# Optimization experiments

Hardware: AMD Instinct MI355X
Metric: run time of the kernel (lower is better)

## Reference

```python
import jax, jax.numpy as jnp
import numpy as np

REG = 0.1  # config['reg']


def _poly_filter(s, gammas):
    # Horner evaluation of sum_k gammas[k] * s**k (monomial basis, depth K=len-1).
    out = jnp.full_like(s, gammas[-1])
    for k in range(gammas.shape[0] - 2, -1, -1):
        out = out * s + gammas[k]
    return out


def setup_inputs() -> dict:
    key = jax.random.key(0)
    k1, k2, k3, k4, k5 = jax.random.split(key, 5)
    B, H, N, R = 4, 8, 4096, 64
    U = jax.random.normal(k1, (B, H, N, R), dtype=jnp.float32)
    Sigma = jax.random.normal(k2, (B, H, 1, R), dtype=jnp.float32)
    svd_V = jax.random.normal(k3, (B, H, N, R), dtype=jnp.float32)
    V = jax.random.normal(k4, (B, H, N, R), dtype=jnp.float32)
    mask = jnp.ones((B, N), dtype=jnp.float32)
    # learnable polynomial coefficients; gamma_0 fixed to 1 (fixI=True)
    gammas = jnp.concatenate([jnp.ones((1,), jnp.float32),
                              0.1 * jax.random.normal(k5, (4,), dtype=jnp.float32)])
    return {"U": U, "Sigma": Sigma, "svd_V": svd_V, "V": V, "mask": mask, "gammas": gammas}


def reference(U, Sigma, svd_V, V, mask, gammas):
    # Q: softmax over rank dim r
    Q = jax.nn.softmax(U, axis=-1)                                      # [B,H,N,r]
    # K: masked softmax over sequence dim N
    Kmat = jax.nn.softmax(svd_V - 1e9 * (1.0 - mask[:, None, :, None]), axis=-2)
    S = jax.nn.sigmoid(Sigma)                                           # [B,H,1,r]
    graph_filter = _poly_filter(S, gammas)                              # [B,H,1,r]
    # linear-attention ordering: (Q*filt) @ (K^T @ V), never forms NxN
    KtV = jnp.einsum('bhnr,bhnd->bhrd', Kmat, V)                        # [B,H,r,d]
    X = jnp.einsum('bhnr,bhrd->bhnd', Q * graph_filter, KtV)            # [B,H,N,d]
    r = Q.shape[-1]
    eye = jnp.eye(r, dtype=Q.dtype)
    symQ = jnp.einsum('bhnr,bhns->bhrs', Q, Q) - eye
    ortho_loss = REG * jnp.mean(jnp.abs(symQ), axis=(1, 2, 3))
    symK = jnp.einsum('bhnr,bhns->bhrs', Kmat, Kmat) - eye
    ortho_loss = ortho_loss + REG * jnp.mean(jnp.abs(symK), axis=(1, 2, 3))
    return X, ortho_loss
```

## Files before the change

### kernel.cpp

```cpp
#include <hip/hip_runtime.h>
#include <math.h>

#define NB 4
#define NH 8
#define BHN 32
#define SN 4096
#define RR 64
#define REGC 0.1f

#define MCH 16
#define MROWS 256
#define XCH 32
#define XROWS 128

typedef short s16x8 __attribute__((ext_vector_type(8)));
typedef float f32x4 __attribute__((ext_vector_type(4)));

__device__ __forceinline__ float wave_sum(float v) {
    #pragma unroll
    for (int off = 32; off; off >>= 1) v += __shfl_xor(v, off, 64);
    return v;
}
__device__ __forceinline__ unsigned short f2bf(float x) {
    unsigned int u = __float_as_uint(x);
    u += 0x7FFFu + ((u >> 16) & 1u);
    return (unsigned short)(u >> 16);
}
__device__ __forceinline__ float bf2f(unsigned short h) {
    return __uint_as_float(((unsigned int)h) << 16);
}
__device__ __forceinline__ unsigned int packbf(float a, float b) {
    return (unsigned int)f2bf(a) | ((unsigned int)f2bf(b) << 16);
}
__device__ __forceinline__ s16x8 ldfrag(const unsigned int* p) {
    uint4 r = *(const uint4*)p;
    return __builtin_bit_cast(s16x8, r);
}
__device__ __forceinline__ int swz(int row, int blk) {
    return (row << 5) + (((blk ^ (row & 7))) << 2);
}
__device__ __forceinline__ void split8(const float* x, uint4& hi, uint4& lo) {
    unsigned short h[8];
    #pragma unroll
    for (int i = 0; i < 8; i++) h[i] = f2bf(x[i]);
    hi = make_uint4((unsigned)h[0] | ((unsigned)h[1] << 16),
                    (unsigned)h[2] | ((unsigned)h[3] << 16),
                    (unsigned)h[4] | ((unsigned)h[5] << 16),
                    (unsigned)h[6] | ((unsigned)h[7] << 16));
    lo = make_uint4(packbf(x[0] - bf2f(h[0]), x[1] - bf2f(h[1])),
                    packbf(x[2] - bf2f(h[2]), x[3] - bf2f(h[3])),
                    packbf(x[4] - bf2f(h[4]), x[5] - bf2f(h[5])),
                    packbf(x[6] - bf2f(h[6]), x[7] - bf2f(h[7])));
}

__global__ void k_zero_loss(float* loss) {
    if (threadIdx.x < NB) loss[threadIdx.x] = 0.0f;
}

#define PH 0
#define VH 2048
#define VL 4096
#define QH 6144
__launch_bounds__(512, 4)
__global__ void k_main(const float* __restrict__ U, const float* __restrict__ sv,
                       const float* __restrict__ V, const float* __restrict__ mask,
                       float* __restrict__ ktv_part, float* __restrict__ symk_part,
                       float* __restrict__ symq_part, float* __restrict__ colsum_part) {
    __shared__ __align__(16) unsigned int sm[16384];
    const int chunk = blockIdx.x, bh = blockIdx.y, b = bh >> 3;
    const int t = threadIdx.x, l = t & 63, w = t >> 6;
    const int r15 = l & 15, quad = l >> 4;
    const int ni = w & 3, mi0 = (w >> 2) << 1;
    const size_t rowbase = (size_t)bh * SN * RR;
    const int row0 = chunk * MROWS;

    float csum = 0.0f;
    f32x4 aKV[2], aSK[2], aSQ[2];
    #pragma unroll
    for (int j = 0; j < 2; j++) {
        aKV[j] = (f32x4){0.f, 0.f, 0.f, 0.f};
        aSK[j] = (f32x4){0.f, 0.f, 0.f, 0.f};
        aSQ[j] = (f32x4){0.f, 0.f, 0.f, 0.f};
    }

    float bu[2][8], bx[2][8], bv[2][8];
    #pragma unroll
    for (int i = 0; i < 8; i++) {
        const size_t off = rowbase + (size_t)(row0 + 8 * w + i) * RR + l;
        bu[0][i] = U[off]; bx[0][i] = sv[off]; bv[0][i] = V[off];
    }

    #pragma unroll
    for (int s = 0; s < 4; s++) {
        const int cur = s & 1, nxt = cur ^ 1;
        const int nb = row0 + s * 64;
        const int bufb = (s & 1) * 8192;
        float bm[8];
        #pragma unroll
        for (int i = 0; i < 8; i++) bm[i] = mask[b * SN + nb + 8 * w + i];
        float q[8], p[8], vv[8];
        #pragma unroll
        for (int i = 0; i < 8; i++) {
            const float eu = __expf(bu[cur][i]);
            q[i] = eu * (1.0f / wave_sum(eu));
        }
        #pragma unroll
        for (int i = 0; i < 8; i++) {
            p[i] = __expf(bx[cur][i] - 1e9f * (1.0f - bm[i]));
            csum += p[i];
            vv[i] = bv[cur][i];
        }
        if (s < 3) {
            #pragma unroll
            for (int i = 0; i < 8; i++) {
                const size_t off = rowbase + (size_t)(nb + 64 + 8 * w + i) * RR + l;
                bu[nxt][i] = U[off]; bx[nxt][i] = sv[off]; bv[nxt][i] = V[off];
            }
        }
        uint4 vh, vl;
        split8(vv, vh, vl);
        const uint4 ph = make_uint4(packbf(p[0], p[1]), packbf(p[2], p[3]),
                                    packbf(p[4], p[5]), packbf(p[6], p[7]));
        const uint4 qh = make_uint4(packbf(q[0], q[1]), packbf(q[2], q[3]),
                                    packbf(q[4], q[5]), packbf(q[6], q[7]));
        const int wbase = bufb + (l << 5) + ((w ^ (l & 7)) << 2);
        *(uint4*)(sm + PH + wbase) = ph;
        *(uint4*)(sm + VH + wbase) = vh;
        *(uint4*)(sm + VL + wbase) = vl;
        *(uint4*)(sm + QH + wbase) = qh;
        __syncthreads();
        #pragma unroll
        for (int ks = 0; ks < 2; ks++) {
            const int ub = ks * 4 + quad;
            s16x8 Ah[2], AQ[2];
            #pragma unroll
            for (int j = 0; j < 2; j++) {
                const int oa = bufb + swz((mi0 + j) * 16 + r15, ub);
                Ah[j] = ldfrag(sm + PH + oa);
                AQ[j] = ldfrag(sm + QH + oa);
            }
            const int ob = bufb + swz(ni * 16 + r15, ub);
            const s16x8 Bvh = ldfrag(sm + VH + ob);
            const s16x8 Bvl = ldfrag(sm + VL + ob);
            const s16x8 Bph = ldfrag(sm + PH + ob);
            const s16x8 Bq  = ldfrag(sm + QH + ob);
            #pragma unroll
            for (int j = 0; j < 2; j++) {
                aKV[j] = __builtin_amdgcn_mfma_f32_16x16x32_bf16(Ah[j], Bvh, aKV[j], 0, 0, 0);
                aKV[j] = __builtin_amdgcn_mfma_f32_16x16x32_bf16(Ah[j], Bvl, aKV[j], 0, 0, 0);
                aSK[j] = __builtin_amdgcn_mfma_f32_16x16x32_bf16(Ah[j], Bph, aSK[j], 0, 0, 0);
                aSQ[j] = __builtin_amdgcn_mfma_f32_16x16x32_bf16(AQ[j], Bq,  aSQ[j], 0, 0, 0);
            }
        }
    }
    const size_t pb = ((size_t)bh * MCH + chunk) * 4096;
    #pragma unroll
    for (int j = 0; j < 2; j++)
        #pragma unroll
        for (int r = 0; r < 4; r++) {
            const int e = ((mi0 + j) * 16 + quad * 4 + r) * 64 + ni * 16 + r15;
            ktv_part[pb + e]  = aKV[j][r];
            symk_part[pb + e] = aSK[j][r];
            symq_part[pb + e] = aSQ[j][r];
        }
    __syncthreads();
    float* smf = (float*)sm;
    smf[w * 64 + l] = csum;
    __syncthreads();
    if (w == 0) {
        float scol = 0.f;
        #pragma unroll
        for (int j = 0; j < 8; j++) scol += smf[j * 64 + l];
        colsum_part[(bh * MCH + chunk) * 64 + l] = scol;
    }
}

__global__ void k_finalize(const float* __restrict__ ktv_part, const float* __restrict__ symk_part,
                           const float* __restrict__ symq_part, const float* __restrict__ colsum_part,
                           const float* __restrict__ Sigma, const float* __restrict__ gammas,
                           unsigned short* __restrict__ ktvt_hi, unsigned short* __restrict__ ktvt_lo,
                           float* __restrict__ loss) {
    const int rb = blockIdx.x, bh = blockIdx.y, b = bh >> 3, t = threadIdx.x;
    __shared__ float cs[64];
    if (t < 64) {
        float s = 0.f;
        for (int c = 0; c < MCH; c++) s += colsum_part[(bh * MCH + c) * 64 + t];
        cs[t] = s;
    }
    __syncthreads();
    const float g0 = gammas[0], g1 = gammas[1], g2 = gammas[2], g3 = gammas[3], g4 = gammas[4];
    float lsum = 0.0f;
    #pragma unroll
    for (int o = 0; o < 2; o++) {
        const int idx = rb * 512 + o * 256 + t;
        const int r = idx >> 6, c = idx & 63;
        float kv = 0.f, sk = 0.f, sq = 0.f;
        for (int ch = 0; ch < MCH; ch++) {
            const size_t pb = ((size_t)bh * MCH + ch) * 4096 + idx;
            kv += ktv_part[pb]; sk += symk_part[pb]; sq += symq_part[pb];
        }
        const float iSr = 1.0f / cs[r], iSc = 1.0f / cs[c];
        kv *= iSr;
        sk *= iSr * iSc;
        const float sg = 1.0f / (1.0f + __expf(-Sigma[bh * 64 + r]));
        float f = g4; f = f * sg + g3; f = f * sg + g2; f = f * sg + g1; f = f * sg + g0;
        const float kvf = kv * f;
        const unsigned short h = f2bf(kvf);
        ktvt_hi[bh * 4096 + c * 64 + r] = h;
        ktvt_lo[bh * 4096 + c * 64 + r] = f2bf(kvf - bf2f(h));
        const float eye = (r == c) ? 1.0f : 0.0f;
        lsum += fabsf(sk - eye) + fabsf(sq - eye);
    }
    lsum = wave_sum(lsum);
    __shared__ float smr[4];
    if ((t & 63) == 0) smr[t >> 6] = lsum;
    __syncthreads();
    if (t == 0)
        atomicAdd(loss + b, (REGC / (NH * 64.0f * 64.0f)) * (smr[0] + smr[1] + smr[2] + smr[3]));
}

__launch_bounds__(512, 8)
__global__ void k_xq(const float* __restrict__ U,
                     const unsigned short* __restrict__ ktvt_hi,
                     const unsigned short* __restrict__ ktvt_lo,
                     float* __restrict__ Xout) {
    __shared__ __align__(16) unsigned int sm[4096];
    const int chunk = blockIdx.x, bh = blockIdx.y;
    const int t = threadIdx.x, l = t & 63, w = t >> 6;
    const int r15 = l & 15, quad = l >> 4;
    const int ni = w & 3, mi0 = (w >> 2) << 1;
    const size_t rowbase = (size_t)bh * SN * RR;
    const int row0 = chunk * XROWS;

    s16x8 Bh[2], Bl[2];
    #pragma unroll
    for (int ks = 0; ks < 2; ks++) {
        const int idx = (ni * 16 + r15) * 64 + ks * 32 + quad * 8;
        Bh[ks] = __builtin_bit_cast(s16x8, *(const uint4*)(ktvt_hi + (size_t)bh * 4096 + idx));
        Bl[ks] = __builtin_bit_cast(s16x8, *(const uint4*)(ktvt_lo + (size_t)bh * 4096 + idx));
    }

    float bu[2][8];
    #pragma unroll
    for (int i = 0; i < 8; i++)
        bu[0][i] = U[rowbase + (size_t)(row0 + 8 * w + i) * RR + l];

    const int jhalf = l >> 1;
    #pragma unroll
    for (int s = 0; s < 2; s++) {
        const int cur = s & 1, nxt = cur ^ 1;
        const int nb = row0 + s * 64;
        const int bufb = (s & 1) * 2048;
        unsigned int wordv[8];
        #pragma unroll
        for (int i = 0; i < 8; i++) {
            const float eu = __expf(bu[cur][i]);
            const float q = eu * (1.0f / wave_sum(eu));
            const float qn = __shfl_xor(q, 1, 64);
            wordv[i] = (unsigned)f2bf(q) | ((unsigned)f2bf(qn) << 16);
        }
        if (s < 1) {
            #pragma unroll
            for (int i = 0; i < 8; i++)
                bu[nxt][i] = U[rowbase + (size_t)(nb + 64 + 8 * w + i) * RR + l];
        }
        #pragma unroll
        for (int i = 0; i < 8; i++) {
            if ((l & 1) == 0) {
                const int nl = 8 * w + i;
                const int addr = (nl << 5) + ((((jhalf >> 2) ^ (nl & 7)) << 2) | (jhalf & 3));
                sm[bufb + addr] = wordv[i];
            }
        }
        __syncthreads();
        f32x4 acc[2];
        acc[0] = (f32x4){0.f, 0.f, 0.f, 0.f};
        acc[1] = (f32x4){0.f, 0.f, 0.f, 0.f};
        #pragma unroll
        for (int ks = 0; ks < 2; ks++) {
            #pragma unroll
            for (int jj = 0; jj < 2; jj++) {
                const int oa = bufb + swz((mi0 + jj) * 16 + r15, ks * 4 + quad);
                const s16x8 Ah = ldfrag(sm + oa);
                acc[jj] = __builtin_amdgcn_mfma_f32_16x16x32_bf16(Ah, Bh[ks], acc[jj], 0, 0, 0);
                acc[jj] = __builtin_amdgcn_mfma_f32_16x16x32_bf16(Ah, Bl[ks], acc[jj], 0, 0, 0);
            }
        }
        #pragma unroll
        for (int jj = 0; jj < 2; jj++)
            #pragma unroll
            for (int r = 0; r < 4; r++) {
                const int n = nb + (mi0 + jj) * 16 + quad * 4 + r;
                Xout[rowbase + (size_t)n * RR + ni * 16 + r15] = acc[jj][r];
            }
    }
}

extern "C" void kernel_launch(void* const* d_in, const int* in_sizes, int n_in,
                              void* d_out, int out_size, void* d_ws, size_t ws_size,
                              hipStream_t stream) {
    (void)in_sizes; (void)n_in; (void)out_size; (void)ws_size;
    const float* U      = (const float*)d_in[0];
    const float* Sigma  = (const float*)d_in[1];
    const float* sv     = (const float*)d_in[2];
    const float* V      = (const float*)d_in[3];
    const float* mask   = (const float*)d_in[4];
    const float* gammas = (const float*)d_in[5];

    float* X    = (float*)d_out;
    float* loss = X + (size_t)BHN * SN * RR;

    float* ws          = (float*)d_ws;
    float* ktv_part    = ws;
    float* symk_part   = ktv_part + (size_t)BHN * MCH * 4096;
    float* symq_part   = symk_part + (size_t)BHN * MCH * 4096;
    float* colsum_part = symq_part + (size_t)BHN * MCH * 4096;
    unsigned short* ktvt_hi = (unsigned short*)(colsum_part + BHN * MCH * 64);
    unsigned short* ktvt_lo = ktvt_hi + BHN * 4096;

    hipLaunchKernelGGL(k_zero_loss, dim3(1), dim3(64), 0, stream, loss);
    hipLaunchKernelGGL(k_main, dim3(MCH, BHN), dim3(512), 0, stream,
                       U, sv, V, mask, ktv_part, symk_part, symq_part, colsum_part);
    hipLaunchKernelGGL(k_finalize, dim3(8, BHN), dim3(256), 0, stream,
                       ktv_part, symk_part, symq_part, colsum_part, Sigma, gammas,
                       ktvt_hi, ktvt_lo, loss);
    hipLaunchKernelGGL(k_xq, dim3(XCH, BHN), dim3(512), 0, stream,
                       U, ktvt_hi, ktvt_lo, X);
}
```

Measured before the change: 164.9 us.

## Drop V hi/lo split, use DPP reductions, vectorize U loads in k_xq

In k_main, V is now packed to a single bf16 term instead of a hi/lo split. This removes one MFMA per tile, one LDS buffer and one fragment load, at some cost in KtV accuracy. The softmax row sum uses DPP row shuffles instead of six shfl_xor steps. In k_xq, each lane now loads 8 contiguous floats as float4 and reduces over an octet of lanes, replacing the per-element wave reductions and the scattered 32-bit LDS writes with one swizzled 16-byte store.

Result: faster. 158.0 us (-4.2%).

```diff
diff --git a/kernel.cpp b/kernel.cpp
--- a/kernel.cpp
+++ b/kernel.cpp
@@ -21,6 +21,21 @@
     for (int off = 32; off; off >>= 1) v += __shfl_xor(v, off, 64);
     return v;
 }
+__device__ __forceinline__ float wave_sum64(float v) {
+    v += __int_as_float(__builtin_amdgcn_update_dpp(0, __float_as_int(v), 0x121, 0xf, 0xf, true));
+    v += __int_as_float(__builtin_amdgcn_update_dpp(0, __float_as_int(v), 0x122, 0xf, 0xf, true));
+    v += __int_as_float(__builtin_amdgcn_update_dpp(0, __float_as_int(v), 0x124, 0xf, 0xf, true));
+    v += __int_as_float(__builtin_amdgcn_update_dpp(0, __float_as_int(v), 0x128, 0xf, 0xf, true));
+    v += __shfl_xor(v, 16, 64);
+    v += __shfl_xor(v, 32, 64);
+    return v;
+}
+__device__ __forceinline__ float octet_sum(float v) {
+    v += __int_as_float(__builtin_amdgcn_update_dpp(0, __float_as_int(v), 0xB1, 0xf, 0xf, true));
+    v += __int_as_float(__builtin_amdgcn_update_dpp(0, __float_as_int(v), 0x4E, 0xf, 0xf, true));
+    v += __shfl_xor(v, 4, 64);
+    return v;
+}
 __device__ __forceinline__ unsigned short f2bf(float x) {
     unsigned int u = __float_as_uint(x);
     u += 0x7FFFu + ((u >> 16) & 1u);
@@ -39,18 +54,9 @@
 __device__ __forceinline__ int swz(int row, int blk) {
     return (row << 5) + (((blk ^ (row & 7))) << 2);
 }
-__device__ __forceinline__ void split8(const float* x, uint4& hi, uint4& lo) {
-    unsigned short h[8];
-    #pragma unroll
-    for (int i = 0; i < 8; i++) h[i] = f2bf(x[i]);
-    hi = make_uint4((unsigned)h[0] | ((unsigned)h[1] << 16),
-                    (unsigned)h[2] | ((unsigned)h[3] << 16),
-                    (unsigned)h[4] | ((unsigned)h[5] << 16),
-                    (unsigned)h[6] | ((unsigned)h[7] << 16));
-    lo = make_uint4(packbf(x[0] - bf2f(h[0]), x[1] - bf2f(h[1])),
-                    packbf(x[2] - bf2f(h[2]), x[3] - bf2f(h[3])),
-                    packbf(x[4] - bf2f(h[4]), x[5] - bf2f(h[5])),
-                    packbf(x[6] - bf2f(h[6]), x[7] - bf2f(h[7])));
+__device__ __forceinline__ uint4 pack8(const float* x) {
+    return make_uint4(packbf(x[0], x[1]), packbf(x[2], x[3]),
+                      packbf(x[4], x[5]), packbf(x[6], x[7]));
 }
 
 __global__ void k_zero_loss(float* loss) {
@@ -59,14 +65,13 @@
 
 #define PH 0
 #define VH 2048
-#define VL 4096
-#define QH 6144
+#define QH 4096
 __launch_bounds__(512, 4)
 __global__ void k_main(const float* __restrict__ U, const float* __restrict__ sv,
                        const float* __restrict__ V, const float* __restrict__ mask,
                        float* __restrict__ ktv_part, float* __restrict__ symk_part,
                        float* __restrict__ symq_part, float* __restrict__ colsum_part) {
-    __shared__ __align__(16) unsigned int sm[16384];
+    __shared__ __align__(16) unsigned int sm[12288];
     const int chunk = blockIdx.x, bh = blockIdx.y, b = bh >> 3;
     const int t = threadIdx.x, l = t & 63, w = t >> 6;
     const int r15 = l & 15, quad = l >> 4;
@@ -94,21 +99,20 @@
     for (int s = 0; s < 4; s++) {
         const int cur = s & 1, nxt = cur ^ 1;
         const int nb = row0 + s * 64;
-        const int bufb = (s & 1) * 8192;
+        const int bufb = cur * 6144;
         float bm[8];
         #pragma unroll
         for (int i = 0; i < 8; i++) bm[i] = mask[b * SN + nb + 8 * w + i];
-        float q[8], p[8], vv[8];
+        float q[8], p[8];
         #pragma unroll
         for (int i = 0; i < 8; i++) {
             const float eu = __expf(bu[cur][i]);
-            q[i] = eu * (1.0f / wave_sum(eu));
+            q[i] = eu * (1.0f / wave_sum64(eu));
         }
         #pragma unroll
         for (int i = 0; i < 8; i++) {
             p[i] = __expf(bx[cur][i] - 1e9f * (1.0f - bm[i]));
             csum += p[i];
-            vv[i] = bv[cur][i];
         }
         if (s < 3) {
             #pragma unroll
@@ -117,16 +121,12 @@
                 bu[nxt][i] = U[off]; bx[nxt][i] = sv[off]; bv[nxt][i] = V[off];
             }
         }
-        uint4 vh, vl;
-        split8(vv, vh, vl);
-        const uint4 ph = make_uint4(packbf(p[0], p[1]), packbf(p[2], p[3]),
-                                    packbf(p[4], p[5]), packbf(p[6], p[7]));
-        const uint4 qh = make_uint4(packbf(q[0], q[1]), packbf(q[2], q[3]),
-                                    packbf(q[4], q[5]), packbf(q[6], q[7]));
+        const uint4 ph = pack8(p);
+        const uint4 vh = pack8(bv[cur]);
+        const uint4 qh = pack8(q);
         const int wbase = bufb + (l << 5) + ((w ^ (l & 7)) << 2);
         *(uint4*)(sm + PH + wbase) = ph;
         *(uint4*)(sm + VH + wbase) = vh;
-        *(uint4*)(sm + VL + wbase) = vl;
         *(uint4*)(sm + QH + wbase) = qh;
         __syncthreads();
         #pragma unroll
@@ -141,13 +141,11 @@
             }
             const int ob = bufb + swz(ni * 16 + r15, ub);
             const s16x8 Bvh = ldfrag(sm + VH + ob);
-            const s16x8 Bvl = ldfrag(sm + VL + ob);
             const s16x8 Bph = ldfrag(sm + PH + ob);
             const s16x8 Bq  = ldfrag(sm + QH + ob);
             #pragma unroll
             for (int j = 0; j < 2; j++) {
                 aKV[j] = __builtin_amdgcn_mfma_f32_16x16x32_bf16(Ah[j], Bvh, aKV[j], 0, 0, 0);
-                aKV[j] = __builtin_amdgcn_mfma_f32_16x16x32_bf16(Ah[j], Bvl, aKV[j], 0, 0, 0);
                 aSK[j] = __builtin_amdgcn_mfma_f32_16x16x32_bf16(Ah[j], Bph, aSK[j], 0, 0, 0);
                 aSQ[j] = __builtin_amdgcn_mfma_f32_16x16x32_bf16(AQ[j], Bq,  aSQ[j], 0, 0, 0);
             }
@@ -231,6 +229,8 @@
     const int ni = w & 3, mi0 = (w >> 2) << 1;
     const size_t rowbase = (size_t)bh * SN * RR;
     const int row0 = chunk * XROWS;
+    const int nl = 8 * w + (l >> 3);
+    const int c0 = (l & 7) * 8;
 
     s16x8 Bh[2], Bl[2];
     #pragma unroll
@@ -240,38 +240,36 @@
         Bl[ks] = __builtin_bit_cast(s16x8, *(const uint4*)(ktvt_lo + (size_t)bh * 4096 + idx));
     }
 
-    float bu[2][8];
-    #pragma unroll
-    for (int i = 0; i < 8; i++)
-        bu[0][i] = U[rowbase + (size_t)(row0 + 8 * w + i) * RR + l];
-
-    const int jhalf = l >> 1;
+    float4 ba[2], bb[2];
+    {
+        const float* src = U + rowbase + (size_t)(row0 + nl) * RR + c0;
+        ba[0] = *(const float4*)src;
+        bb[0] = *(const float4*)(src + 4);
+    }
+
     #pragma unroll
     for (int s = 0; s < 2; s++) {
         const int cur = s & 1, nxt = cur ^ 1;
         const int nb = row0 + s * 64;
-        const int bufb = (s & 1) * 2048;
-        unsigned int wordv[8];
-        #pragma unroll
-        for (int i = 0; i < 8; i++) {
-            const float eu = __expf(bu[cur][i]);
-            const float q = eu * (1.0f / wave_sum(eu));
-            const float qn = __shfl_xor(q, 1, 64);
-            wordv[i] = (unsigned)f2bf(q) | ((unsigned)f2bf(qn) << 16);
-        }
+        const int bufb = cur * 2048;
+        float e[8];
+        e[0] = __expf(ba[cur].x); e[1] = __expf(ba[cur].y);
+        e[2] = __expf(ba[cur].z); e[3] = __expf(ba[cur].w);
+        e[4] = __expf(bb[cur].x); e[5] = __expf(bb[cur].y);
+        e[6] = __expf(bb[cur].z); e[7] = __expf(bb[cur].w);
+        float loc = 0.f;
+        #pragma unroll
+        for (int i = 0; i < 8; i++) loc += e[i];
+        const float inv = 1.0f / octet_sum(loc);
         if (s < 1) {
-            #pragma unroll
-            for (int i = 0; i < 8; i++)
-                bu[nxt][i] = U[rowbase + (size_t)(nb + 64 + 8 * w + i) * RR + l];
-        }
-        #pragma unroll
-        for (int i = 0; i < 8; i++) {
-            if ((l & 1) == 0) {
-                const int nl = 8 * w + i;
-                const int addr = (nl << 5) + ((((jhalf >> 2) ^ (nl & 7)) << 2) | (jhalf & 3));
-                sm[bufb + addr] = wordv[i];
-            }
-        }
+            const float* src = U + rowbase + (size_t)(nb + 64 + nl) * RR + c0;
+            ba[nxt] = *(const float4*)src;
+            bb[nxt] = *(const float4*)(src + 4);
+        }
+        float q[8];
+        #pragma unroll
+        for (int i = 0; i < 8; i++) q[i] = e[i] * inv;
+        *(uint4*)(sm + bufb + swz(nl, l & 7)) = pack8(q);
         __syncthreads();
         f32x4 acc[2];
         acc[0] = (f32x4){0.f, 0.f, 0.f, 0.f};
```
